# Optimization experiments

Hardware: AMD Instinct MI355X
Metric: run time of the kernel (lower is better)

## Reference

```python
import jax, jax.numpy as jnp
import numpy as np

B, D, L, H = 2, 64, 512, 1024  # batch, n_docs (timesteps), tokens per doc, bert hidden


def _ln(x, g, b):
    # torch.nn.LayerNorm over last dim, eps=1e-5
    m = jnp.mean(x, axis=-1, keepdims=True)
    v = jnp.mean((x - m) ** 2, axis=-1, keepdims=True)
    return (x - m) / jnp.sqrt(v + 1e-5) * g + b


def _ht(x):
    # Hardtanh(min=-8, max=8)
    return jnp.clip(x, -8.0, 8.0)


def setup_inputs() -> dict:
    key = jax.random.key(0)
    ks = jax.random.split(key, 12)
    xavier = lambda k, shape: jax.random.normal(k, shape, dtype=jnp.float32) * np.float32(np.sqrt(2.0 / sum(shape)))
    return {
        "trans": jax.random.normal(ks[0], (B, D, L, H), dtype=jnp.float32) * 0.1,  # frozen BERT last_hidden_state
        "document_mask": jax.random.bernoulli(ks[1], 0.9, (B, D)),
        "Wf": xavier(ks[2], (H, H)), "bf": jnp.ones((H,), jnp.float32),
        "Wi": xavier(ks[3], (H, H)), "bi": jnp.zeros((H,), jnp.float32),
        "Wg": xavier(ks[4], (H, H)), "bg": jnp.zeros((H,), jnp.float32),
        "Wo": xavier(ks[5], (H, H)), "bo": jnp.zeros((H,), jnp.float32),
        "Wp": xavier(ks[6], (H, H)), "bp": jnp.zeros((H,), jnp.float32),
        "tF": xavier(ks[7], (L,)), "tI": xavier(ks[8], (L,)), "tO": xavier(ks[9], (L,)),
        "c_gamma": jnp.ones((H,), jnp.float32), "c_beta": jnp.zeros((H,), jnp.float32),
        "h_gamma": jnp.ones((H,), jnp.float32), "h_beta": jnp.zeros((H,), jnp.float32),
    }


def _forward(trans, document_mask, Wf, bf, Wi, bi, Wg, bg, Wo, bo, Wp, bp,
             tF, tI, tO, c_gamma, c_beta, h_gamma, h_beta):
    b, d, l, h = trans.shape
    # docFlat @ transform: contract the token (l) axis -> [b, d, h]
    pF = jnp.einsum('bdlh,l->bdh', trans, tF)
    pI = jnp.einsum('bdlh,l->bdh', trans, tI)
    pO = jnp.einsum('bdlh,l->bdh', trans, tO)

    def step(carry, xs):
        c, hs = carry                      # each [b, h]
        pf, pi, po, m = xs                 # [b, h] x3, [b] bool
        nC = _ln(c, c_gamma, c_beta)
        nH = _ln(hs, h_gamma, h_beta)
        f = jax.nn.sigmoid(_ht(nH @ Wf.T + bf) + pf)
        c2 = c * f
        i = jax.nn.sigmoid(_ht(nH @ Wi.T + bi) + pi)
        g = _ht(jax.nn.gelu(nH @ Wg.T + bg, approximate=False) + pi)
        c2 = c2 + i * g
        o = jax.nn.sigmoid(_ht(nH @ Wo.T + bo) + po)
        h2 = o * _ht(jax.nn.gelu(nC @ Wp.T + bp, approximate=False))
        mm = m[:, None]
        h2 = jnp.where(mm, h2, hs)
        c2 = jnp.where(mm, c2, c)
        c2 = jnp.clip(c2, -10.0, 10.0)
        h2 = jnp.clip(h2, -10.0, 10.0)
        return (c2, h2), None

    init = (jnp.zeros((b, h), trans.dtype), jnp.zeros((b, h), trans.dtype))
    xs = (pF.transpose(1, 0, 2), pI.transpose(1, 0, 2), pO.transpose(1, 0, 2), document_mask.T)
    (c_fin, h_fin), _ = jax.lax.scan(step, init, xs)
    return h_fin  # [b, h] (original returns [b, h, 1])


def reference(trans, document_mask, Wf, bf, Wi, bi, Wg, bg, Wo, bo, Wp, bp,
              tF, tI, tO, c_gamma, c_beta, h_gamma, h_beta):
    return _forward(trans, document_mask, Wf, bf, Wi, bi, Wg, bg, Wo, bo, Wp, bp,
                    tF, tI, tO, c_gamma, c_beta, h_gamma, h_beta)
```

## Files before the change

### kernel.cpp

```cpp
#include <hip/hip_runtime.h>
#include <math.h>


#define NBLK 256

__device__ __forceinline__ float sigf(float x)   { return 1.0f / (1.0f + __expf(-x)); }
__device__ __forceinline__ float geluf(float x)  { return 0.5f * x * (1.0f + erff(x * 0.70710678118654752f)); }
__device__ __forceinline__ float clampf(float x, float lo, float hi) { return fminf(fmaxf(x, lo), hi); }

__device__ __forceinline__ void astf(float* p, float v) {
    __hip_atomic_store(p, v, __ATOMIC_RELAXED, __HIP_MEMORY_SCOPE_AGENT);
}
__device__ __forceinline__ float aldf(const float* p) {
    return __hip_atomic_load(p, __ATOMIC_RELAXED, __HIP_MEMORY_SCOPE_AGENT);
}
__device__ __forceinline__ void astu(unsigned* p, unsigned v) {
    __hip_atomic_store(p, v, __ATOMIC_RELAXED, __HIP_MEMORY_SCOPE_AGENT);
}
__device__ __forceinline__ unsigned aldu(const unsigned* p) {
    return __hip_atomic_load(p, __ATOMIC_RELAXED, __HIP_MEMORY_SCOPE_AGENT);
}

__global__ __launch_bounds__(256, 1) void fused_kernel(
    const float* __restrict__ trans, const int* __restrict__ mask,
    const float* __restrict__ Wf, const float* __restrict__ bf,
    const float* __restrict__ Wi, const float* __restrict__ bi,
    const float* __restrict__ Wg, const float* __restrict__ bg,
    const float* __restrict__ Wo, const float* __restrict__ bo,
    const float* __restrict__ Wp, const float* __restrict__ bp,
    const float* __restrict__ tF, const float* __restrict__ tI, const float* __restrict__ tO,
    const float* __restrict__ c_gamma, const float* __restrict__ c_beta,
    const float* __restrict__ h_gamma, const float* __restrict__ h_beta,
    float* __restrict__ ws, float* __restrict__ out)
{
    const int t    = threadIdx.x;
    const int lane = t & 63;
    const int wv   = t >> 6;
    const int blk  = blockIdx.x;
    const int hrow = (blk << 2) + wv;

    unsigned* flags = (unsigned*)ws;
    float* stC = ws + 320;
    float* stH = ws + 4416;
    float* pF  = ws + 8512;
    float* pI  = pF + 131072;
    float* pO  = pI + 131072;

    __shared__ float smem[2][4][1024];
    __shared__ float red[2][4][8];

    float4 wfr[4], wir[4], wgr[4], wor[4], wpr[4];
    {
        const float4* rf = (const float4*)(Wf + (size_t)hrow * 1024);
        const float4* ri = (const float4*)(Wi + (size_t)hrow * 1024);
        const float4* rg = (const float4*)(Wg + (size_t)hrow * 1024);
        const float4* ro = (const float4*)(Wo + (size_t)hrow * 1024);
        const float4* rp = (const float4*)(Wp + (size_t)hrow * 1024);
        #pragma unroll
        for (int q = 0; q < 4; ++q) {
            const int k4 = lane + 64 * q;
            wfr[q] = rf[k4]; wir[q] = ri[k4]; wgr[q] = rg[k4];
            wor[q] = ro[k4]; wpr[q] = rp[k4];
        }
    }
    const float bfv = bf[hrow], biv = bi[hrow], bgv = bg[hrow], bov = bo[hrow], bpv = bp[hrow];

    {
        float* sF = &smem[0][0][0];
        float* sI = &smem[0][0][512];
        float* sO = &smem[0][1][0];
        sF[t] = tF[t]; sF[t + 256] = tF[t + 256];
        sI[t] = tI[t]; sI[t + 256] = tI[t + 256];
        sO[t] = tO[t]; sO[t + 256] = tO[t + 256];
        __syncthreads();

        const int bd = blk >> 1;
        const int h0 = (blk & 1) * 512;
        const int s  = t & 127;
        const int g  = t >> 7;
        const float4* tr = (const float4*)trans + (size_t)bd * 512 * 256 + (h0 >> 2) + s;

        float4 aF = make_float4(0.f,0.f,0.f,0.f);
        float4 aI = make_float4(0.f,0.f,0.f,0.f);
        float4 aO = make_float4(0.f,0.f,0.f,0.f);
        #pragma unroll 8
        for (int li = 0; li < 256; ++li) {
            const int l = g + 2 * li;
            float4 v = tr[(size_t)l * 256];
            const float wf = sF[l], wi = sI[l], wo = sO[l];
            aF.x = fmaf(v.x, wf, aF.x); aF.y = fmaf(v.y, wf, aF.y);
            aF.z = fmaf(v.z, wf, aF.z); aF.w = fmaf(v.w, wf, aF.w);
            aI.x = fmaf(v.x, wi, aI.x); aI.y = fmaf(v.y, wi, aI.y);
            aI.z = fmaf(v.z, wi, aI.z); aI.w = fmaf(v.w, wi, aI.w);
            aO.x = fmaf(v.x, wo, aO.x); aO.y = fmaf(v.y, wo, aO.y);
            aO.z = fmaf(v.z, wo, aO.z); aO.w = fmaf(v.w, wo, aO.w);
        }
        float4* cmb = (float4*)&smem[0][2][0];
        if (g == 1) { cmb[s] = aF; cmb[128 + s] = aI; cmb[256 + s] = aO; }
        __syncthreads();
        if (g == 0) {
            const float4 bF = cmb[s], bI = cmb[128 + s], bO = cmb[256 + s];
            aF.x += bF.x; aF.y += bF.y; aF.z += bF.z; aF.w += bF.w;
            aI.x += bI.x; aI.y += bI.y; aI.z += bI.z; aI.w += bI.w;
            aO.x += bO.x; aO.y += bO.y; aO.z += bO.z; aO.w += bO.w;
            const int base = bd * 1024 + h0 + 4 * s;
            astf(&pF[base+0], aF.x); astf(&pF[base+1], aF.y);
            astf(&pF[base+2], aF.z); astf(&pF[base+3], aF.w);
            astf(&pI[base+0], aI.x); astf(&pI[base+1], aI.y);
            astf(&pI[base+2], aI.z); astf(&pI[base+3], aI.w);
            astf(&pO[base+0], aO.x); astf(&pO[base+1], aO.y);
            astf(&pO[base+2], aO.z); astf(&pO[base+3], aO.w);
        }
    }
    __syncthreads();
    if (t == 0) astu(&flags[blk], 1u);

    float sfv, siv, sgv, sov, spv, bfb, bib, bgb, bob, bpb;
    {
        float4 gh4[4], bh4[4], gc4[4], bc4[4];
        const float4* Gh = (const float4*)h_gamma;
        const float4* Bh = (const float4*)h_beta;
        const float4* Gc = (const float4*)c_gamma;
        const float4* Bc = (const float4*)c_beta;
        #pragma unroll
        for (int q = 0; q < 4; ++q) {
            const int k4 = lane + 64 * q;
            gh4[q] = Gh[k4]; bh4[q] = Bh[k4]; gc4[q] = Gc[k4]; bc4[q] = Bc[k4];
        }
        bfb = bib = bgb = bob = bpb = 0.f;
        #pragma unroll
        for (int q = 0; q < 4; ++q) {
            bfb += wfr[q].x*bh4[q].x + wfr[q].y*bh4[q].y + wfr[q].z*bh4[q].z + wfr[q].w*bh4[q].w;
            bib += wir[q].x*bh4[q].x + wir[q].y*bh4[q].y + wir[q].z*bh4[q].z + wir[q].w*bh4[q].w;
            bgb += wgr[q].x*bh4[q].x + wgr[q].y*bh4[q].y + wgr[q].z*bh4[q].z + wgr[q].w*bh4[q].w;
            bob += wor[q].x*bh4[q].x + wor[q].y*bh4[q].y + wor[q].z*bh4[q].z + wor[q].w*bh4[q].w;
            bpb += wpr[q].x*bc4[q].x + wpr[q].y*bc4[q].y + wpr[q].z*bc4[q].z + wpr[q].w*bc4[q].w;
        }
        #pragma unroll
        for (int q = 0; q < 4; ++q) {
            wfr[q].x *= gh4[q].x; wfr[q].y *= gh4[q].y; wfr[q].z *= gh4[q].z; wfr[q].w *= gh4[q].w;
            wir[q].x *= gh4[q].x; wir[q].y *= gh4[q].y; wir[q].z *= gh4[q].z; wir[q].w *= gh4[q].w;
            wgr[q].x *= gh4[q].x; wgr[q].y *= gh4[q].y; wgr[q].z *= gh4[q].z; wgr[q].w *= gh4[q].w;
            wor[q].x *= gh4[q].x; wor[q].y *= gh4[q].y; wor[q].z *= gh4[q].z; wor[q].w *= gh4[q].w;
            wpr[q].x *= gc4[q].x; wpr[q].y *= gc4[q].y; wpr[q].z *= gc4[q].z; wpr[q].w *= gc4[q].w;
        }
        sfv = siv = sgv = sov = spv = 0.f;
        #pragma unroll
        for (int q = 0; q < 4; ++q) {
            sfv += wfr[q].x + wfr[q].y + wfr[q].z + wfr[q].w;
            siv += wir[q].x + wir[q].y + wir[q].z + wir[q].w;
            sgv += wgr[q].x + wgr[q].y + wgr[q].z + wgr[q].w;
            sov += wor[q].x + wor[q].y + wor[q].z + wor[q].w;
            spv += wpr[q].x + wpr[q].y + wpr[q].z + wpr[q].w;
        }
        #pragma unroll
        for (int off = 32; off; off >>= 1) {
            sfv += __shfl_xor(sfv, off); siv += __shfl_xor(siv, off);
            sgv += __shfl_xor(sgv, off); sov += __shfl_xor(sov, off);
            spv += __shfl_xor(spv, off);
            bfb += __shfl_xor(bfb, off); bib += __shfl_xor(bib, off);
            bgb += __shfl_xor(bgb, off); bob += __shfl_xor(bob, off);
            bpb += __shfl_xor(bpb, off);
        }
    }

    if (wv == 0) {
        for (;;) {
            const unsigned a0 = aldu(&flags[lane]);
            const unsigned a1 = aldu(&flags[lane + 64]);
            const unsigned a2 = aldu(&flags[lane + 128]);
            const unsigned a3 = aldu(&flags[lane + 192]);
            const int ok = (a0 >= 1u) && (a1 >= 1u) && (a2 >= 1u) && (a3 >= 1u);
            if (__all(ok)) break;
            __builtin_amdgcn_s_sleep(1);
        }
    }
    __syncthreads();

    float c_prev = 0.f, h_prev = 0.f;

    for (int d = 0; d < 64; ++d) {
        const int par = d & 1;
        const float* cc = stC + par * 2048;
        const float* hc = stH + par * 2048;
        float* cn = stC + (par ^ 1) * 2048;
        float* hn = stH + (par ^ 1) * 2048;
        float (*sm)[1024] = smem[par];
        float (*rd)[8]    = red[par];

        float pfv = 0.f, piv = 0.f, pov = 0.f;
        int mv = 1;
        if (lane < 2) {
            const int pidx = (lane * 64 + d) * 1024 + hrow;
            pfv = aldf(&pF[pidx]); piv = aldf(&pI[pidx]); pov = aldf(&pO[pidx]);
            mv = mask[lane * 64 + d];
        }

        if (wv == 0) {
            const unsigned tgt = (unsigned)(d + 1);
            for (;;) {
                const unsigned a0 = aldu(&flags[lane]);
                const unsigned a1 = aldu(&flags[lane + 64]);
                const unsigned a2 = aldu(&flags[lane + 128]);
                const unsigned a3 = aldu(&flags[lane + 192]);
                const int ok = (a0 >= tgt) && (a1 >= tgt) && (a2 >= tgt) && (a3 >= tgt);
                if (__all(ok)) break;
                __builtin_amdgcn_s_sleep(1);
            }
        }
        __syncthreads();

        float cv0[4], cv1[4], hv0[4], hv1[4];
        #pragma unroll
        for (int j = 0; j < 4; ++j) {
            const int e = t + 256 * j;
            cv0[j] = aldf(cc + e);        cv1[j] = aldf(cc + 1024 + e);
            hv0[j] = aldf(hc + e);        hv1[j] = aldf(hc + 1024 + e);
        }
        float s0=0,s1=0,s2=0,s3=0,s4=0,s5=0,s6=0,s7=0;
        #pragma unroll
        for (int j = 0; j < 4; ++j) {
            const int e = t + 256 * j;
            sm[0][e] = hv0[j]; sm[1][e] = hv1[j];
            sm[2][e] = cv0[j]; sm[3][e] = cv1[j];
            s0 += cv0[j]; s1 += cv0[j]*cv0[j];
            s2 += cv1[j]; s3 += cv1[j]*cv1[j];
            s4 += hv0[j]; s5 += hv0[j]*hv0[j];
            s6 += hv1[j]; s7 += hv1[j]*hv1[j];
        }
        #pragma unroll
        for (int off = 32; off; off >>= 1) {
            s0 += __shfl_xor(s0, off); s1 += __shfl_xor(s1, off);
            s2 += __shfl_xor(s2, off); s3 += __shfl_xor(s3, off);
            s4 += __shfl_xor(s4, off); s5 += __shfl_xor(s5, off);
            s6 += __shfl_xor(s6, off); s7 += __shfl_xor(s7, off);
        }
        if (lane == 0) {
            rd[wv][0]=s0; rd[wv][1]=s1; rd[wv][2]=s2; rd[wv][3]=s3;
            rd[wv][4]=s4; rd[wv][5]=s5; rd[wv][6]=s6; rd[wv][7]=s7;
        }
        __syncthreads();

        const float tc0 = rd[0][0]+rd[1][0]+rd[2][0]+rd[3][0];
        const float qc0 = rd[0][1]+rd[1][1]+rd[2][1]+rd[3][1];
        const float tc1 = rd[0][2]+rd[1][2]+rd[2][2]+rd[3][2];
        const float qc1 = rd[0][3]+rd[1][3]+rd[2][3]+rd[3][3];
        const float th0 = rd[0][4]+rd[1][4]+rd[2][4]+rd[3][4];
        const float qh0 = rd[0][5]+rd[1][5]+rd[2][5]+rd[3][5];
        const float th1 = rd[0][6]+rd[1][6]+rd[2][6]+rd[3][6];
        const float qh1 = rd[0][7]+rd[1][7]+rd[2][7]+rd[3][7];
        const float inv = 1.0f / 1024.0f;
        const float mc0 = tc0*inv, rc0 = rsqrtf(qc0*inv - mc0*mc0 + 1e-5f);
        const float mc1 = tc1*inv, rc1 = rsqrtf(qc1*inv - mc1*mc1 + 1e-5f);
        const float mh0 = th0*inv, rh0 = rsqrtf(qh0*inv - mh0*mh0 + 1e-5f);
        const float mh1 = th1*inv, rh1 = rsqrtf(qh1*inv - mh1*mh1 + 1e-5f);

        float zf0=0,zf1=0,zi0=0,zi1=0,zg0=0,zg1=0,zo0=0,zo1=0,zp0=0,zp1=0;
        #pragma unroll
        for (int q = 0; q < 4; ++q) {
            const int k4 = lane + 64 * q;
            const float4 n0 = ((const float4*)sm[0])[k4];
            const float4 n1 = ((const float4*)sm[1])[k4];
            const float4 m0 = ((const float4*)sm[2])[k4];
            const float4 m1 = ((const float4*)sm[3])[k4];
            zf0 += wfr[q].x*n0.x + wfr[q].y*n0.y + wfr[q].z*n0.z + wfr[q].w*n0.w;
            zf1 += wfr[q].x*n1.x + wfr[q].y*n1.y + wfr[q].z*n1.z + wfr[q].w*n1.w;
            zi0 += wir[q].x*n0.x + wir[q].y*n0.y + wir[q].z*n0.z + wir[q].w*n0.w;
            zi1 += wir[q].x*n1.x + wir[q].y*n1.y + wir[q].z*n1.z + wir[q].w*n1.w;
            zg0 += wgr[q].x*n0.x + wgr[q].y*n0.y + wgr[q].z*n0.z + wgr[q].w*n0.w;
            zg1 += wgr[q].x*n1.x + wgr[q].y*n1.y + wgr[q].z*n1.z + wgr[q].w*n1.w;
            zo0 += wor[q].x*n0.x + wor[q].y*n0.y + wor[q].z*n0.z + wor[q].w*n0.w;
            zo1 += wor[q].x*n1.x + wor[q].y*n1.y + wor[q].z*n1.z + wor[q].w*n1.w;
            zp0 += wpr[q].x*m0.x + wpr[q].y*m0.y + wpr[q].z*m0.z + wpr[q].w*m0.w;
            zp1 += wpr[q].x*m1.x + wpr[q].y*m1.y + wpr[q].z*m1.z + wpr[q].w*m1.w;
        }
        #pragma unroll
        for (int off = 32; off; off >>= 1) {
            zf0 += __shfl_xor(zf0, off); zf1 += __shfl_xor(zf1, off);
            zi0 += __shfl_xor(zi0, off); zi1 += __shfl_xor(zi1, off);
            zg0 += __shfl_xor(zg0, off); zg1 += __shfl_xor(zg1, off);
            zo0 += __shfl_xor(zo0, off); zo1 += __shfl_xor(zo1, off);
            zp0 += __shfl_xor(zp0, off); zp1 += __shfl_xor(zp1, off);
        }

        if (lane < 2) {
            const int b = lane;
            const float mh = b ? mh1 : mh0, rh = b ? rh1 : rh0;
            const float mc = b ? mc1 : mc0, rc = b ? rc1 : rc0;
            const float zf = rh * ((b ? zf1 : zf0) - mh * sfv) + bfb;
            const float zi = rh * ((b ? zi1 : zi0) - mh * siv) + bib;
            const float zg = rh * ((b ? zg1 : zg0) - mh * sgv) + bgb;
            const float zo = rh * ((b ? zo1 : zo0) - mh * sov) + bob;
            const float zp = rc * ((b ? zp1 : zp0) - mc * spv) + bpb;
            const float f  = sigf(clampf(zf + bfv, -8.f, 8.f) + pfv);
            const float ig = sigf(clampf(zi + biv, -8.f, 8.f) + piv);
            const float g  = clampf(geluf(zg + bgv) + piv, -8.f, 8.f);
            const float o  = sigf(clampf(zo + bov, -8.f, 8.f) + pov);
            const float hp = clampf(geluf(zp + bpv), -8.f, 8.f);
            float c2 = c_prev * f + ig * g;
            float h2 = o * hp;
            if (mv == 0) { c2 = c_prev; h2 = h_prev; }
            c2 = clampf(c2, -10.f, 10.f);
            h2 = clampf(h2, -10.f, 10.f);
            c_prev = c2; h_prev = h2;
            if (d == 63) {
                out[b * 1024 + hrow] = h2;
            } else {
                astf(cn + b * 1024 + hrow, c2);
                astf(hn + b * 1024 + hrow, h2);
            }
        }

        if (d == 63) break;
        __syncthreads();
        if (t == 0) astu(&flags[blk], (unsigned)(d + 2));
    }
}

extern "C" void kernel_launch(void* const* d_in, const int* in_sizes, int n_in,
                              void* d_out, int out_size, void* d_ws, size_t ws_size,
                              hipStream_t stream)
{
    const float* trans = (const float*)d_in[0];
    const int*   mask  = (const int*)d_in[1];
    const float* Wf = (const float*)d_in[2];  const float* bf = (const float*)d_in[3];
    const float* Wi = (const float*)d_in[4];  const float* bi = (const float*)d_in[5];
    const float* Wg = (const float*)d_in[6];  const float* bg = (const float*)d_in[7];
    const float* Wo = (const float*)d_in[8];  const float* bo = (const float*)d_in[9];
    const float* Wp = (const float*)d_in[10]; const float* bp = (const float*)d_in[11];
    const float* tF = (const float*)d_in[12];
    const float* tI = (const float*)d_in[13];
    const float* tO = (const float*)d_in[14];
    const float* c_gamma = (const float*)d_in[15];
    const float* c_beta  = (const float*)d_in[16];
    const float* h_gamma = (const float*)d_in[17];
    const float* h_beta  = (const float*)d_in[18];

    float* ws  = (float*)d_ws;
    float* out = (float*)d_out;

    hipMemsetAsync(d_ws, 0, 8512u * sizeof(float), stream);

    void* args[] = { (void*)&trans, (void*)&mask,
                     (void*)&Wf, (void*)&bf, (void*)&Wi, (void*)&bi,
                     (void*)&Wg, (void*)&bg, (void*)&Wo, (void*)&bo,
                     (void*)&Wp, (void*)&bp,
                     (void*)&tF, (void*)&tI, (void*)&tO,
                     (void*)&c_gamma, (void*)&c_beta, (void*)&h_gamma, (void*)&h_beta,
                     (void*)&ws, (void*)&out };
    hipLaunchCooperativeKernel((void*)fused_kernel, dim3(256), dim3(256), args, 0, stream);
}
```

Before: 895.7 us.

## Use hierarchical release flags and fold LayerNorm stats into matvec reduction

```diff
diff --git a/kernel.cpp b/kernel.cpp
--- a/kernel.cpp
+++ b/kernel.cpp
@@ -40,14 +40,14 @@
     const int hrow = (blk << 2) + wv;
 
     unsigned* flags = (unsigned*)ws;
-    float* stC = ws + 320;
-    float* stH = ws + 4416;
-    float* pF  = ws + 8512;
+    unsigned* rel   = flags + 256;
+    float* stC = ws + 512;
+    float* stH = ws + 4608;
+    float* pF  = ws + 8704;
     float* pI  = pF + 131072;
     float* pO  = pI + 131072;
 
     __shared__ float smem[2][4][1024];
-    __shared__ float red[2][4][8];
 
     float4 wfr[4], wir[4], wgr[4], wor[4], wpr[4];
     {
@@ -164,16 +164,21 @@
         }
     }
 
-    if (wv == 0) {
-        for (;;) {
-            const unsigned a0 = aldu(&flags[lane]);
-            const unsigned a1 = aldu(&flags[lane + 64]);
-            const unsigned a2 = aldu(&flags[lane + 128]);
-            const unsigned a3 = aldu(&flags[lane + 192]);
-            const int ok = (a0 >= 1u) && (a1 >= 1u) && (a2 >= 1u) && (a3 >= 1u);
-            if (__all(ok)) break;
-            __builtin_amdgcn_s_sleep(1);
-        }
+    if (blk == 0) {
+        if (wv == 0) {
+            for (;;) {
+                const unsigned a0 = aldu(&flags[lane]);
+                const unsigned a1 = aldu(&flags[lane + 64]);
+                const unsigned a2 = aldu(&flags[lane + 128]);
+                const unsigned a3 = aldu(&flags[lane + 192]);
+                const int ok = (a0 >= 1u) && (a1 >= 1u) && (a2 >= 1u) && (a3 >= 1u);
+                if (__all(ok)) break;
+                __builtin_amdgcn_s_sleep(1);
+            }
+            if (lane < 16) astu(&rel[lane * 16], 1u);
+        }
+    } else if (t == 0) {
+        while (aldu(&rel[(blk & 15) * 16]) < 1u) __builtin_amdgcn_s_sleep(2);
     }
     __syncthreads();
 
@@ -186,7 +191,6 @@
         float* cn = stC + (par ^ 1) * 2048;
         float* hn = stH + (par ^ 1) * 2048;
         float (*sm)[1024] = smem[par];
-        float (*rd)[8]    = red[par];
 
         float pfv = 0.f, piv = 0.f, pov = 0.f;
         int mv = 1;
@@ -196,66 +200,44 @@
             mv = mask[lane * 64 + d];
         }
 
-        if (wv == 0) {
+        {
             const unsigned tgt = (unsigned)(d + 1);
-            for (;;) {
-                const unsigned a0 = aldu(&flags[lane]);
-                const unsigned a1 = aldu(&flags[lane + 64]);
-                const unsigned a2 = aldu(&flags[lane + 128]);
-                const unsigned a3 = aldu(&flags[lane + 192]);
-                const int ok = (a0 >= tgt) && (a1 >= tgt) && (a2 >= tgt) && (a3 >= tgt);
-                if (__all(ok)) break;
-                __builtin_amdgcn_s_sleep(1);
+            if (blk == 0) {
+                if (wv == 0) {
+                    for (;;) {
+                        const unsigned a0 = aldu(&flags[lane]);
+                        const unsigned a1 = aldu(&flags[lane + 64]);
+                        const unsigned a2 = aldu(&flags[lane + 128]);
+                        const unsigned a3 = aldu(&flags[lane + 192]);
+                        const int ok = (a0 >= tgt) && (a1 >= tgt) && (a2 >= tgt) && (a3 >= tgt);
+                        if (__all(ok)) break;
+                        __builtin_amdgcn_s_sleep(1);
+                    }
+                    if (lane < 16) astu(&rel[lane * 16], tgt);
+                }
+            } else if (t == 0) {
+                while (aldu(&rel[(blk & 15) * 16]) < tgt) __builtin_amdgcn_s_sleep(2);
             }
-        }
-        __syncthreads();
-
-        float cv0[4], cv1[4], hv0[4], hv1[4];
+            __syncthreads();
+        }
+
+        float lh0[4], lh1[4], lc0[4], lc1[4];
         #pragma unroll
         for (int j = 0; j < 4; ++j) {
             const int e = t + 256 * j;
-            cv0[j] = aldf(cc + e);        cv1[j] = aldf(cc + 1024 + e);
-            hv0[j] = aldf(hc + e);        hv1[j] = aldf(hc + 1024 + e);
-        }
-        float s0=0,s1=0,s2=0,s3=0,s4=0,s5=0,s6=0,s7=0;
+            lh0[j] = aldf(hc + e);        lh1[j] = aldf(hc + 1024 + e);
+            lc0[j] = aldf(cc + e);        lc1[j] = aldf(cc + 1024 + e);
+        }
         #pragma unroll
         for (int j = 0; j < 4; ++j) {
             const int e = t + 256 * j;
-            sm[0][e] = hv0[j]; sm[1][e] = hv1[j];
-            sm[2][e] = cv0[j]; sm[3][e] = cv1[j];
-            s0 += cv0[j]; s1 += cv0[j]*cv0[j];
-            s2 += cv1[j]; s3 += cv1[j]*cv1[j];
-            s4 += hv0[j]; s5 += hv0[j]*hv0[j];
-            s6 += hv1[j]; s7 += hv1[j]*hv1[j];
-        }
-        #pragma unroll
-        for (int off = 32; off; off >>= 1) {
-            s0 += __shfl_xor(s0, off); s1 += __shfl_xor(s1, off);
-            s2 += __shfl_xor(s2, off); s3 += __shfl_xor(s3, off);
-            s4 += __shfl_xor(s4, off); s5 += __shfl_xor(s5, off);
-            s6 += __shfl_xor(s6, off); s7 += __shfl_xor(s7, off);
-        }
-        if (lane == 0) {
-            rd[wv][0]=s0; rd[wv][1]=s1; rd[wv][2]=s2; rd[wv][3]=s3;
-            rd[wv][4]=s4; rd[wv][5]=s5; rd[wv][6]=s6; rd[wv][7]=s7;
+            sm[0][e] = lh0[j]; sm[1][e] = lh1[j];
+            sm[2][e] = lc0[j]; sm[3][e] = lc1[j];
         }
         __syncthreads();
 
-        const float tc0 = rd[0][0]+rd[1][0]+rd[2][0]+rd[3][0];
-        const float qc0 = rd[0][1]+rd[1][1]+rd[2][1]+rd[3][1];
-        const float tc1 = rd[0][2]+rd[1][2]+rd[2][2]+rd[3][2];
-        const float qc1 = rd[0][3]+rd[1][3]+rd[2][3]+rd[3][3];
-        const float th0 = rd[0][4]+rd[1][4]+rd[2][4]+rd[3][4];
-        const float qh0 = rd[0][5]+rd[1][5]+rd[2][5]+rd[3][5];
-        const float th1 = rd[0][6]+rd[1][6]+rd[2][6]+rd[3][6];
-        const float qh1 = rd[0][7]+rd[1][7]+rd[2][7]+rd[3][7];
-        const float inv = 1.0f / 1024.0f;
-        const float mc0 = tc0*inv, rc0 = rsqrtf(qc0*inv - mc0*mc0 + 1e-5f);
-        const float mc1 = tc1*inv, rc1 = rsqrtf(qc1*inv - mc1*mc1 + 1e-5f);
-        const float mh0 = th0*inv, rh0 = rsqrtf(qh0*inv - mh0*mh0 + 1e-5f);
-        const float mh1 = th1*inv, rh1 = rsqrtf(qh1*inv - mh1*mh1 + 1e-5f);
-
         float zf0=0,zf1=0,zi0=0,zi1=0,zg0=0,zg1=0,zo0=0,zo1=0,zp0=0,zp1=0;
+        float sH0=0,qH0=0,sH1=0,qH1=0,sC0=0,qC0=0,sC1=0,qC1=0;
         #pragma unroll
         for (int q = 0; q < 4; ++q) {
             const int k4 = lane + 64 * q;
@@ -273,6 +255,14 @@
             zo1 += wor[q].x*n1.x + wor[q].y*n1.y + wor[q].z*n1.z + wor[q].w*n1.w;
             zp0 += wpr[q].x*m0.x + wpr[q].y*m0.y + wpr[q].z*m0.z + wpr[q].w*m0.w;
             zp1 += wpr[q].x*m1.x + wpr[q].y*m1.y + wpr[q].z*m1.z + wpr[q].w*m1.w;
+            sH0 += n0.x + n0.y + n0.z + n0.w;
+            qH0 += n0.x*n0.x + n0.y*n0.y + n0.z*n0.z + n0.w*n0.w;
+            sH1 += n1.x + n1.y + n1.z + n1.w;
+            qH1 += n1.x*n1.x + n1.y*n1.y + n1.z*n1.z + n1.w*n1.w;
+            sC0 += m0.x + m0.y + m0.z + m0.w;
+            qC0 += m0.x*m0.x + m0.y*m0.y + m0.z*m0.z + m0.w*m0.w;
+            sC1 += m1.x + m1.y + m1.z + m1.w;
+            qC1 += m1.x*m1.x + m1.y*m1.y + m1.z*m1.z + m1.w*m1.w;
         }
         #pragma unroll
         for (int off = 32; off; off >>= 1) {
@@ -281,12 +271,21 @@
             zg0 += __shfl_xor(zg0, off); zg1 += __shfl_xor(zg1, off);
             zo0 += __shfl_xor(zo0, off); zo1 += __shfl_xor(zo1, off);
             zp0 += __shfl_xor(zp0, off); zp1 += __shfl_xor(zp1, off);
+            sH0 += __shfl_xor(sH0, off); qH0 += __shfl_xor(qH0, off);
+            sH1 += __shfl_xor(sH1, off); qH1 += __shfl_xor(qH1, off);
+            sC0 += __shfl_xor(sC0, off); qC0 += __shfl_xor(qC0, off);
+            sC1 += __shfl_xor(sC1, off); qC1 += __shfl_xor(qC1, off);
         }
 
         if (lane < 2) {
             const int b = lane;
-            const float mh = b ? mh1 : mh0, rh = b ? rh1 : rh0;
-            const float mc = b ? mc1 : mc0, rc = b ? rc1 : rc0;
+            const float inv = 1.0f / 1024.0f;
+            const float mh = (b ? sH1 : sH0) * inv;
+            const float qh = (b ? qH1 : qH0) * inv;
+            const float rh = rsqrtf(qh - mh * mh + 1e-5f);
+            const float mc = (b ? sC1 : sC0) * inv;
+            const float qc = (b ? qC1 : qC0) * inv;
+            const float rc = rsqrtf(qc - mc * mc + 1e-5f);
             const float zf = rh * ((b ? zf1 : zf0) - mh * sfv) + bfb;
             const float zi = rh * ((b ? zi1 : zi0) - mh * siv) + bib;
             const float zg = rh * ((b ? zg1 : zg0) - mh * sgv) + bgb;
@@ -339,7 +338,7 @@
     float* ws  = (float*)d_ws;
     float* out = (float*)d_out;
 
-    hipMemsetAsync(d_ws, 0, 8512u * sizeof(float), stream);
+    hipMemsetAsync(d_ws, 0, 8704u * sizeof(float), stream);
 
     void* args[] = { (void*)&trans, (void*)&mask,
                      (void*)&Wf, (void*)&bf, (void*)&Wi, (void*)&bi,
```

Result: faster. 801.9 us (-10.5%).
